# Kernel tuning notes

Hardware: AMD Instinct MI355X
Metric: run time of the kernel (lower is better)

The kernel has to match this reference:

```python
import jax, jax.numpy as jnp
import numpy as np

CONF_THRES = 0.7
IOU_THRES = 0.45
TOP_K = 1000  # max candidates kept per image after confidence filtering (YOLOv5 max_nms-style cap)
IMG_SIZE = 640.0


def _box_iou(boxes):
    """Pairwise IoU of [K,4] xyxy boxes -> [K,K]."""
    area = (boxes[:, 2] - boxes[:, 0]) * (boxes[:, 3] - boxes[:, 1])
    lt = jnp.maximum(boxes[:, None, :2], boxes[None, :, :2])
    rb = jnp.minimum(boxes[:, None, 2:], boxes[None, :, 2:])
    wh = jnp.clip(rb - lt, 0.0)
    inter = wh[..., 0] * wh[..., 1]
    return inter / (area[:, None] + area[None, :] - inter + 1e-7)


def _nms_single(pred):
    """YOLOv5-style NMS for one image. pred: [N, 9] = xywh, obj, cls_conf, pitch, yaw, roll.
    Returns fixed-shape padded detections [TOP_K, 9] and keep mask [TOP_K]."""
    obj = pred[:, 4]
    conf = obj * pred[:, 5]  # nc=1: conf = obj_conf * cls_conf
    valid = (obj > CONF_THRES) & (conf > CONF_THRES)
    score = jnp.where(valid, conf, -1.0)

    top_scores, idx = jax.lax.top_k(score, TOP_K)
    p = pred[idx]  # [TOP_K, 9]
    xy, wh = p[:, :2], p[:, 2:4]
    boxes = jnp.concatenate([xy - wh * 0.5, xy + wh * 0.5], axis=-1)  # xywh -> xyxy

    keep0 = top_scores > CONF_THRES
    iou = _box_iou(boxes)  # [TOP_K, TOP_K]
    ar = jnp.arange(TOP_K)

    # Greedy NMS: boxes are score-sorted; box j is suppressed if a kept earlier box overlaps > thresh.
    def body(i, keep):
        sup = (iou[i] > IOU_THRES) & (ar > i) & keep[i]
        return keep & (~sup)

    keep = jax.lax.fori_loop(0, TOP_K, body, keep0)

    cls = jnp.zeros((TOP_K, 1), boxes.dtype)  # single class (head)
    out = jnp.concatenate([boxes, top_scores[:, None], cls, p[:, 6:9]], axis=-1)  # [TOP_K, 9]
    out = out * keep[:, None].astype(out.dtype)  # zero padded/suppressed rows
    return out, keep


def setup_inputs() -> dict:
    key = jax.random.key(0)
    B, N = 32, 25200
    r = jax.random.uniform(key, (B, N, 9), dtype=jnp.float32)
    xy = r[..., :2] * IMG_SIZE                 # box centers in pixels
    wh = r[..., 2:4] * 128.0 + 4.0             # box sizes 4..132 px
    obj = r[..., 4:5]                          # objectness in [0,1)
    cls = r[..., 5:6] * 0.5 + 0.5              # class conf in [0.5,1)
    ang = (r[..., 6:9] - 0.5) * 2.0            # normalized pitch/yaw/roll
    prediction = jnp.concatenate([xy, wh, obj, cls, ang], axis=-1)
    return {"prediction": prediction}


def reference(prediction):
    out, keep = jax.vmap(_nms_single)(prediction)
    return out, keep
```

## Files before the change

### kernel.cpp

```cpp
#include <hip/hip_runtime.h>
#include <stdint.h>

#pragma clang fp contract(off)

#define BATCH 32
#define NPRED 25200
#define ROWF 9
#define TOPK 1000
#define SUBS 8
#define ROWS_PER_SUB (NPRED / SUBS)
#define SUBCAP 512
#define CONF_T 0.7f
#define IOU_T 0.45f
#define KW 16
#define SUPROW 1024
#define TKROW 1024

typedef unsigned long long u64;
typedef unsigned int u32;

#define WS_CAND 0
#define WS_TKEY (1048576)
#define WS_SUP  (WS_TKEY + 262144)

__device__ __forceinline__ u64 readlane64(u64 v, int l) {
    u32 lo = __builtin_amdgcn_readlane((u32)v, (u32)l);
    u32 hi = __builtin_amdgcn_readlane((u32)(v >> 32), (u32)l);
    return ((u64)hi << 32) | lo;
}

__global__ __launch_bounds__(512) void compact_sort_kernel(const float* __restrict__ pred,
                                                           u64* __restrict__ cand_ws,
                                                           u64* __restrict__ tkey_ws) {
    __shared__ float stage[512 * ROWF];
    __shared__ u64 skey[SUBCAP];
    __shared__ u32 cnt;
    int bs = blockIdx.x;
    int b = bs >> 3, s = bs & 7;
    int tid = threadIdx.x;
    if (tid == 0) cnt = 0;
    skey[tid] = 0;
    if (tid < 128) tkey_ws[bs * 128 + tid] = 0;
    __syncthreads();
    int r0 = s * ROWS_PER_SUB;
    for (int c0 = 0; c0 < ROWS_PER_SUB; c0 += 512) {
        int nrows = ROWS_PER_SUB - c0; if (nrows > 512) nrows = 512;
        int nfl = nrows * ROWF;
        size_t g0 = ((size_t)b * NPRED + r0 + c0) * ROWF;
        int h = (int)((4 - (g0 & 3)) & 3); if (h > nfl) h = nfl;
        if (tid < h) stage[tid] = pred[g0 + tid];
        int nv = (nfl - h) >> 2;
        const float4* pv = (const float4*)(pred + g0 + h);
        for (int v = tid; v < nv; v += 512) {
            float4 q = pv[v];
            int d = h + v * 4;
            stage[d] = q.x; stage[d + 1] = q.y; stage[d + 2] = q.z; stage[d + 3] = q.w;
        }
        for (int t2 = h + nv * 4 + tid; t2 < nfl; t2 += 512) stage[t2] = pred[g0 + t2];
        __syncthreads();
        if (tid < nrows) {
            float obj = stage[tid * ROWF + 4];
            float cls = stage[tid * ROWF + 5];
            float conf = obj * cls;
            if (obj > CONF_T && conf > CONF_T) {
                int r = r0 + c0 + tid;
                u32 slot = atomicAdd(&cnt, 1u);
                if (slot < SUBCAP)
                    skey[slot] = ((u64)__float_as_uint(conf) << 32) | (u64)(u32)(~(u32)r);
            }
        }
        __syncthreads();
    }
    for (int k = 2; k <= SUBCAP; k <<= 1) {
        for (int j = k >> 1; j > 0; j >>= 1) {
            int t = tid, p = t ^ j;
            if (p > t) {
                u64 a = skey[t], c2 = skey[p];
                bool desc = ((t & k) == 0);
                if (desc ? (a < c2) : (a > c2)) { skey[t] = c2; skey[p] = a; }
            }
            __syncthreads();
        }
    }
    cand_ws[(size_t)bs * SUBCAP + tid] = skey[tid];
}

__global__ __launch_bounds__(512) void rank_kernel(const u64* __restrict__ cand_ws,
                                                   u64* __restrict__ tkey_ws) {
    __shared__ u64 lists[SUBS * SUBCAP];
    int bs = blockIdx.x;
    int b = bs >> 3, s = bs & 7;
    int tid = threadIdx.x;
    const u64* src = cand_ws + (size_t)b * SUBS * SUBCAP;
    for (int t = tid; t < SUBS * SUBCAP; t += 512) lists[t] = src[t];
    __syncthreads();
    u64 key = lists[(s << 9) + tid];
    if (key) {
        int lo[SUBS];
#pragma unroll
        for (int l = 0; l < SUBS; ++l) lo[l] = 0;
#pragma unroll
        for (int w2 = SUBCAP; w2 >= 1; w2 >>= 1) {
#pragma unroll
            for (int l = 0; l < SUBS; ++l) {
                int p = lo[l] + w2;
                if (p <= SUBCAP && lists[(l << 9) + p - 1] > key) lo[l] = p;
            }
        }
        int rank = 0;
#pragma unroll
        for (int l = 0; l < SUBS; ++l) rank += lo[l];
        if (rank < TOPK) tkey_ws[(size_t)b * TKROW + rank] = key;
    }
}

__global__ __launch_bounds__(1024) void supmat_kernel(const float* __restrict__ pred,
                                                      const u64* __restrict__ tkey_ws,
                                                      u64* __restrict__ sup_g) {
    __shared__ float4 bx_s[TOPK];
    __shared__ float  ar_s[TOPK];
    int b = blockIdx.x >> 3, q = blockIdx.x & 7;
    int tid = threadIdx.x;
    if (tid < TOPK) {
        u64 key = tkey_ws[(size_t)b * TKROW + tid];
        float4 box = make_float4(0.f, 0.f, 0.f, 0.f);
        float ar = 0.f;
        if (key) {
            u32 r = ~(u32)key;
            const float* p = pred + ((size_t)b * NPRED + r) * ROWF;
            float x = p[0], y = p[1], w = p[2], hh = p[3];
            box = make_float4(x - w * 0.5f, y - hh * 0.5f, x + w * 0.5f, y + hh * 0.5f);
            ar = (box.z - box.x) * (box.w - box.y);
        }
        bx_s[tid] = box; ar_s[tid] = ar;
    }
    __syncthreads();
    int wave = tid >> 6, lane = tid & 63;
    for (int pass = 0; pass < 2; ++pass) {
        int t = (pass == 0) ? (q * 16 + wave) : ((wave == 15) ? 128 + q : 136);
        if (t >= 136) continue;
        int iw = 0, rem = t, c = 16;
        while (rem >= c) { rem -= c; c--; iw++; }
        int jw = iw + rem;
        int i = iw * 64 + lane;
        bool act = i < TOPK;
        float4 bi = act ? bx_s[i] : make_float4(0.f, 0.f, 0.f, 0.f);
        float ai = act ? ar_s[i] : 0.f;
        u64 m = 0;
        int jbase = jw << 6;
        int jend = jbase + 64; if (jend > TOPK) jend = TOPK;
        for (int j = jbase; j < jend; ++j) {
            float4 bj = bx_s[j];
            float aj = ar_s[j];
            float lx = fmaxf(bi.x, bj.x);
            float ly = fmaxf(bi.y, bj.y);
            float rx = fminf(bi.z, bj.z);
            float ry = fminf(bi.w, bj.w);
            float iw2 = rx - lx; iw2 = iw2 > 0.f ? iw2 : 0.f;
            float ih = ry - ly; ih = ih > 0.f ? ih : 0.f;
            float inter = iw2 * ih;
            float den = ai + aj - inter + 1e-7f;
            float iou = inter / den;
            if (act && j > i && iou > IOU_T) m |= 1ull << (j - jbase);
        }
        if (act) sup_g[((size_t)b * KW + jw) * SUPROW + i] = m;
    }
}

__global__ __launch_bounds__(1024) void scan_out_kernel(const float* __restrict__ pred,
                                                        const u64* __restrict__ tkey_ws,
                                                        const u64* __restrict__ sup_g,
                                                        float* __restrict__ out,
                                                        float* __restrict__ keepout) {
    __shared__ u64 keep_lds[KW];
    __shared__ u64 acc_lds;
    int b = blockIdx.x, tid = threadIdx.x;
    int w = tid >> 6, lane = tid & 63;
    const u64* S = sup_g + (size_t)b * KW * SUPROW;

    u64 key = tkey_ws[(size_t)b * TKROW + tid];
    u64 keep0 = __ballot(key != 0ull);
    if (lane == 0) keep_lds[w] = keep0;

    u64 sup_reg[KW];
    u64 diagreg = 0;
#pragma unroll
    for (int bi = 0; bi < KW; ++bi) {
        sup_reg[bi] = S[(size_t)w * SUPROW + (bi << 6) + lane];
        if (bi == w) diagreg = sup_reg[bi];
    }
    __syncthreads();

    u64 nzmask = __ballot(diagreg != 0);

#pragma unroll
    for (int bi = 0; bi < KW; ++bi) {
        if (w == bi) {
            u64 cur = keep_lds[bi];
            u64 active = cur & nzmask;
            while (active) {
                int i = __ffsll((long long)active) - 1;
                u64 wi = readlane64(diagreg, i);
                active &= active - 1;
                cur &= ~wi;
                active &= ~wi;
            }
            if (lane == 0) { keep_lds[bi] = cur; acc_lds = cur; }
        }
        __syncthreads();
        if (w > bi) {
            u64 A = acc_lds;
            u64 myv = sup_reg[bi];
            bool accb = (A >> lane) & 1ull;
            u64 lanes = __ballot(accb && myv != 0ull);
            if (lanes) {
                u64 wred = 0;
                while (lanes) {
                    int l = __ffsll((long long)lanes) - 1;
                    wred |= readlane64(myv, l);
                    lanes &= lanes - 1;
                }
                if (lane == 0) keep_lds[w] &= ~wred;
            }
        }
        __syncthreads();
    }

    if (tid < TOPK) {
        bool kp = ((keep_lds[w] >> lane) & 1ull) != 0;
        float o0 = 0.f, o1 = 0.f, o2 = 0.f, o3 = 0.f, o4 = 0.f, o6 = 0.f, o7 = 0.f, o8 = 0.f;
        if (kp) {
            u32 r = ~(u32)key;
            const float* p = pred + ((size_t)b * NPRED + r) * ROWF;
            float x = p[0], y = p[1], wd = p[2], hh = p[3];
            o0 = x - wd * 0.5f; o1 = y - hh * 0.5f;
            o2 = x + wd * 0.5f; o3 = y + hh * 0.5f;
            o4 = __uint_as_float((u32)(key >> 32));
            o6 = p[6]; o7 = p[7]; o8 = p[8];
        }
        size_t ob = ((size_t)b * TOPK + tid) * ROWF;
        out[ob + 0] = o0; out[ob + 1] = o1; out[ob + 2] = o2; out[ob + 3] = o3;
        out[ob + 4] = o4; out[ob + 5] = 0.f;
        out[ob + 6] = o6; out[ob + 7] = o7; out[ob + 8] = o8;
        keepout[(size_t)b * TOPK + tid] = kp ? 1.0f : 0.0f;
    }
}

extern "C" void kernel_launch(void* const* d_in, const int* in_sizes, int n_in,
                              void* d_out, int out_size, void* d_ws, size_t ws_size,
                              hipStream_t stream) {
    const float* pred = (const float*)d_in[0];
    float* out = (float*)d_out;
    float* keepout = out + (size_t)BATCH * TOPK * ROWF;
    char* ws = (char*)d_ws;
    u64* cand_ws = (u64*)(ws + WS_CAND);
    u64* tkey_ws = (u64*)(ws + WS_TKEY);
    u64* sup_g = (u64*)(ws + WS_SUP);

    compact_sort_kernel<<<BATCH * SUBS, 512, 0, stream>>>(pred, cand_ws, tkey_ws);
    rank_kernel<<<BATCH * SUBS, 512, 0, stream>>>(cand_ws, tkey_ws);
    supmat_kernel<<<BATCH * SUBS, 1024, 0, stream>>>(pred, tkey_ws, sup_g);
    scan_out_kernel<<<BATCH, 1024, 0, stream>>>(pred, tkey_ws, sup_g, out, keepout);
}
```

Measured before the change: 131.7 us.

## Fuse four NMS stages into one cooperative kernel with grid syncs

Merges the compaction/sort, rank-merge, suppression-matrix and greedy-scan kernels into a single cooperative launch of 256 blocks of 512 threads, separated by grid-wide barriers. Shared memory is reused across the phases, and the suppression and scan phases are remapped to 512 threads (each wave handles two 64-column chunks). The goal is to remove the inter-kernel launch gaps and the tail effects between stages. In exchange, the scan phase runs with half the threads per block, and grid.sync barriers plus cooperative launch add their own overhead.

```diff
diff --git a/kernel.cpp b/kernel.cpp
--- a/kernel.cpp
+++ b/kernel.cpp
@@ -1,5 +1,8 @@
 #include <hip/hip_runtime.h>
+#include <hip/hip_cooperative_groups.h>
 #include <stdint.h>
+
+namespace cg = cooperative_groups;
 
 #pragma clang fp contract(off)
 
@@ -29,220 +32,249 @@
     return ((u64)hi << 32) | lo;
 }
 
-__global__ __launch_bounds__(512) void compact_sort_kernel(const float* __restrict__ pred,
-                                                           u64* __restrict__ cand_ws,
-                                                           u64* __restrict__ tkey_ws) {
-    __shared__ float stage[512 * ROWF];
-    __shared__ u64 skey[SUBCAP];
+__global__ __launch_bounds__(512) void mega_kernel(const float* __restrict__ pred,
+                                                   u64* __restrict__ cand_ws,
+                                                   u64* __restrict__ tkey_ws,
+                                                   u64* __restrict__ sup_g,
+                                                   float* __restrict__ out,
+                                                   float* __restrict__ keepout) {
+    cg::grid_group grid = cg::this_grid();
+    __shared__ u64 smem[SUBS * SUBCAP];
     __shared__ u32 cnt;
+    __shared__ u64 acc_lds;
+    __shared__ u64 keep_sh[KW];
+
     int bs = blockIdx.x;
     int b = bs >> 3, s = bs & 7;
     int tid = threadIdx.x;
-    if (tid == 0) cnt = 0;
-    skey[tid] = 0;
-    if (tid < 128) tkey_ws[bs * 128 + tid] = 0;
-    __syncthreads();
-    int r0 = s * ROWS_PER_SUB;
-    for (int c0 = 0; c0 < ROWS_PER_SUB; c0 += 512) {
-        int nrows = ROWS_PER_SUB - c0; if (nrows > 512) nrows = 512;
-        int nfl = nrows * ROWF;
-        size_t g0 = ((size_t)b * NPRED + r0 + c0) * ROWF;
-        int h = (int)((4 - (g0 & 3)) & 3); if (h > nfl) h = nfl;
-        if (tid < h) stage[tid] = pred[g0 + tid];
-        int nv = (nfl - h) >> 2;
-        const float4* pv = (const float4*)(pred + g0 + h);
-        for (int v = tid; v < nv; v += 512) {
-            float4 q = pv[v];
-            int d = h + v * 4;
-            stage[d] = q.x; stage[d + 1] = q.y; stage[d + 2] = q.z; stage[d + 3] = q.w;
-        }
-        for (int t2 = h + nv * 4 + tid; t2 < nfl; t2 += 512) stage[t2] = pred[g0 + t2];
-        __syncthreads();
-        if (tid < nrows) {
-            float obj = stage[tid * ROWF + 4];
-            float cls = stage[tid * ROWF + 5];
-            float conf = obj * cls;
-            if (obj > CONF_T && conf > CONF_T) {
-                int r = r0 + c0 + tid;
-                u32 slot = atomicAdd(&cnt, 1u);
-                if (slot < SUBCAP)
-                    skey[slot] = ((u64)__float_as_uint(conf) << 32) | (u64)(u32)(~(u32)r);
-            }
-        }
-        __syncthreads();
-    }
-    for (int k = 2; k <= SUBCAP; k <<= 1) {
-        for (int j = k >> 1; j > 0; j >>= 1) {
-            int t = tid, p = t ^ j;
-            if (p > t) {
-                u64 a = skey[t], c2 = skey[p];
-                bool desc = ((t & k) == 0);
-                if (desc ? (a < c2) : (a > c2)) { skey[t] = c2; skey[p] = a; }
-            }
-            __syncthreads();
-        }
-    }
-    cand_ws[(size_t)bs * SUBCAP + tid] = skey[tid];
-}
-
-__global__ __launch_bounds__(512) void rank_kernel(const u64* __restrict__ cand_ws,
-                                                   u64* __restrict__ tkey_ws) {
-    __shared__ u64 lists[SUBS * SUBCAP];
-    int bs = blockIdx.x;
-    int b = bs >> 3, s = bs & 7;
-    int tid = threadIdx.x;
-    const u64* src = cand_ws + (size_t)b * SUBS * SUBCAP;
-    for (int t = tid; t < SUBS * SUBCAP; t += 512) lists[t] = src[t];
-    __syncthreads();
-    u64 key = lists[(s << 9) + tid];
-    if (key) {
-        int lo[SUBS];
-#pragma unroll
-        for (int l = 0; l < SUBS; ++l) lo[l] = 0;
-#pragma unroll
-        for (int w2 = SUBCAP; w2 >= 1; w2 >>= 1) {
-#pragma unroll
-            for (int l = 0; l < SUBS; ++l) {
-                int p = lo[l] + w2;
-                if (p <= SUBCAP && lists[(l << 9) + p - 1] > key) lo[l] = p;
-            }
-        }
-        int rank = 0;
-#pragma unroll
-        for (int l = 0; l < SUBS; ++l) rank += lo[l];
-        if (rank < TOPK) tkey_ws[(size_t)b * TKROW + rank] = key;
-    }
-}
-
-__global__ __launch_bounds__(1024) void supmat_kernel(const float* __restrict__ pred,
-                                                      const u64* __restrict__ tkey_ws,
-                                                      u64* __restrict__ sup_g) {
-    __shared__ float4 bx_s[TOPK];
-    __shared__ float  ar_s[TOPK];
-    int b = blockIdx.x >> 3, q = blockIdx.x & 7;
-    int tid = threadIdx.x;
-    if (tid < TOPK) {
-        u64 key = tkey_ws[(size_t)b * TKROW + tid];
-        float4 box = make_float4(0.f, 0.f, 0.f, 0.f);
-        float ar = 0.f;
+
+    {
+        float* stage = (float*)smem;
+        u64* skey = smem + 2304;
+        if (tid == 0) cnt = 0;
+        skey[tid] = 0;
+        if (tid < 128) tkey_ws[bs * 128 + tid] = 0;
+        __syncthreads();
+        int r0 = s * ROWS_PER_SUB;
+        for (int c0 = 0; c0 < ROWS_PER_SUB; c0 += 512) {
+            int nrows = ROWS_PER_SUB - c0; if (nrows > 512) nrows = 512;
+            int nfl = nrows * ROWF;
+            size_t g0 = ((size_t)b * NPRED + r0 + c0) * ROWF;
+            int h = (int)((4 - (g0 & 3)) & 3); if (h > nfl) h = nfl;
+            if (tid < h) stage[tid] = pred[g0 + tid];
+            int nv = (nfl - h) >> 2;
+            const float4* pv = (const float4*)(pred + g0 + h);
+            for (int v = tid; v < nv; v += 512) {
+                float4 q = pv[v];
+                int d = h + v * 4;
+                stage[d] = q.x; stage[d + 1] = q.y; stage[d + 2] = q.z; stage[d + 3] = q.w;
+            }
+            for (int t2 = h + nv * 4 + tid; t2 < nfl; t2 += 512) stage[t2] = pred[g0 + t2];
+            __syncthreads();
+            if (tid < nrows) {
+                float obj = stage[tid * ROWF + 4];
+                float cls = stage[tid * ROWF + 5];
+                float conf = obj * cls;
+                if (obj > CONF_T && conf > CONF_T) {
+                    int r = r0 + c0 + tid;
+                    u32 slot = atomicAdd(&cnt, 1u);
+                    if (slot < SUBCAP)
+                        skey[slot] = ((u64)__float_as_uint(conf) << 32) | (u64)(u32)(~(u32)r);
+                }
+            }
+            __syncthreads();
+        }
+        for (int k = 2; k <= SUBCAP; k <<= 1) {
+            for (int j = k >> 1; j > 0; j >>= 1) {
+                int t = tid, p = t ^ j;
+                if (p > t) {
+                    u64 a = skey[t], c2 = skey[p];
+                    bool desc = ((t & k) == 0);
+                    if (desc ? (a < c2) : (a > c2)) { skey[t] = c2; skey[p] = a; }
+                }
+                __syncthreads();
+            }
+        }
+        cand_ws[(size_t)bs * SUBCAP + tid] = skey[tid];
+    }
+    __threadfence();
+    grid.sync();
+
+    {
+        u64* lists = smem;
+        const u64* src = cand_ws + (size_t)b * SUBS * SUBCAP;
+        for (int t = tid; t < SUBS * SUBCAP; t += 512) lists[t] = src[t];
+        __syncthreads();
+        u64 key = lists[(s << 9) + tid];
         if (key) {
-            u32 r = ~(u32)key;
-            const float* p = pred + ((size_t)b * NPRED + r) * ROWF;
-            float x = p[0], y = p[1], w = p[2], hh = p[3];
-            box = make_float4(x - w * 0.5f, y - hh * 0.5f, x + w * 0.5f, y + hh * 0.5f);
-            ar = (box.z - box.x) * (box.w - box.y);
-        }
-        bx_s[tid] = box; ar_s[tid] = ar;
-    }
-    __syncthreads();
-    int wave = tid >> 6, lane = tid & 63;
-    for (int pass = 0; pass < 2; ++pass) {
-        int t = (pass == 0) ? (q * 16 + wave) : ((wave == 15) ? 128 + q : 136);
-        if (t >= 136) continue;
-        int iw = 0, rem = t, c = 16;
-        while (rem >= c) { rem -= c; c--; iw++; }
-        int jw = iw + rem;
-        int i = iw * 64 + lane;
-        bool act = i < TOPK;
-        float4 bi = act ? bx_s[i] : make_float4(0.f, 0.f, 0.f, 0.f);
-        float ai = act ? ar_s[i] : 0.f;
-        u64 m = 0;
-        int jbase = jw << 6;
-        int jend = jbase + 64; if (jend > TOPK) jend = TOPK;
-        for (int j = jbase; j < jend; ++j) {
-            float4 bj = bx_s[j];
-            float aj = ar_s[j];
-            float lx = fmaxf(bi.x, bj.x);
-            float ly = fmaxf(bi.y, bj.y);
-            float rx = fminf(bi.z, bj.z);
-            float ry = fminf(bi.w, bj.w);
-            float iw2 = rx - lx; iw2 = iw2 > 0.f ? iw2 : 0.f;
-            float ih = ry - ly; ih = ih > 0.f ? ih : 0.f;
-            float inter = iw2 * ih;
-            float den = ai + aj - inter + 1e-7f;
-            float iou = inter / den;
-            if (act && j > i && iou > IOU_T) m |= 1ull << (j - jbase);
-        }
-        if (act) sup_g[((size_t)b * KW + jw) * SUPROW + i] = m;
-    }
-}
-
-__global__ __launch_bounds__(1024) void scan_out_kernel(const float* __restrict__ pred,
-                                                        const u64* __restrict__ tkey_ws,
-                                                        const u64* __restrict__ sup_g,
-                                                        float* __restrict__ out,
-                                                        float* __restrict__ keepout) {
-    __shared__ u64 keep_lds[KW];
-    __shared__ u64 acc_lds;
-    int b = blockIdx.x, tid = threadIdx.x;
-    int w = tid >> 6, lane = tid & 63;
-    const u64* S = sup_g + (size_t)b * KW * SUPROW;
-
-    u64 key = tkey_ws[(size_t)b * TKROW + tid];
-    u64 keep0 = __ballot(key != 0ull);
-    if (lane == 0) keep_lds[w] = keep0;
-
-    u64 sup_reg[KW];
-    u64 diagreg = 0;
-#pragma unroll
-    for (int bi = 0; bi < KW; ++bi) {
-        sup_reg[bi] = S[(size_t)w * SUPROW + (bi << 6) + lane];
-        if (bi == w) diagreg = sup_reg[bi];
-    }
-    __syncthreads();
-
-    u64 nzmask = __ballot(diagreg != 0);
-
-#pragma unroll
-    for (int bi = 0; bi < KW; ++bi) {
-        if (w == bi) {
-            u64 cur = keep_lds[bi];
-            u64 active = cur & nzmask;
-            while (active) {
-                int i = __ffsll((long long)active) - 1;
-                u64 wi = readlane64(diagreg, i);
-                active &= active - 1;
-                cur &= ~wi;
-                active &= ~wi;
-            }
-            if (lane == 0) { keep_lds[bi] = cur; acc_lds = cur; }
-        }
-        __syncthreads();
-        if (w > bi) {
+            int lo[SUBS];
+#pragma unroll
+            for (int l = 0; l < SUBS; ++l) lo[l] = 0;
+#pragma unroll
+            for (int w2 = SUBCAP; w2 >= 1; w2 >>= 1) {
+#pragma unroll
+                for (int l = 0; l < SUBS; ++l) {
+                    int p = lo[l] + w2;
+                    if (p <= SUBCAP && lists[(l << 9) + p - 1] > key) lo[l] = p;
+                }
+            }
+            int rank = 0;
+#pragma unroll
+            for (int l = 0; l < SUBS; ++l) rank += lo[l];
+            if (rank < TOPK) tkey_ws[(size_t)b * TKROW + rank] = key;
+        }
+    }
+    __threadfence();
+    grid.sync();
+
+    {
+        float4* bx_s = (float4*)smem;
+        float* ar_s = (float*)(smem + 2000);
+        for (int t = tid; t < TOPK; t += 512) {
+            u64 key = tkey_ws[(size_t)b * TKROW + t];
+            float4 box = make_float4(0.f, 0.f, 0.f, 0.f);
+            float ar = 0.f;
+            if (key) {
+                u32 r = ~(u32)key;
+                const float* p = pred + ((size_t)b * NPRED + r) * ROWF;
+                float x = p[0], y = p[1], w = p[2], hh = p[3];
+                box = make_float4(x - w * 0.5f, y - hh * 0.5f, x + w * 0.5f, y + hh * 0.5f);
+                ar = (box.z - box.x) * (box.w - box.y);
+            }
+            bx_s[t] = box; ar_s[t] = ar;
+        }
+        __syncthreads();
+        int w = tid >> 6, lane = tid & 63;
+        int gw = (s << 3) + w;
+        for (int ti = 0; ti < 3; ++ti) {
+            int t = gw + (ti << 6);
+            if (t >= 136) break;
+            int iw = 0, rem = t, c = 16;
+            while (rem >= c) { rem -= c; c--; iw++; }
+            int jw = iw + rem;
+            int i = iw * 64 + lane;
+            bool act = i < TOPK;
+            float4 bi = act ? bx_s[i] : make_float4(0.f, 0.f, 0.f, 0.f);
+            float ai = act ? ar_s[i] : 0.f;
+            u64 m = 0;
+            int jbase = jw << 6;
+            int jend = jbase + 64; if (jend > TOPK) jend = TOPK;
+            for (int j = jbase; j < jend; ++j) {
+                float4 bj = bx_s[j];
+                float aj = ar_s[j];
+                float lx = fmaxf(bi.x, bj.x);
+                float ly = fmaxf(bi.y, bj.y);
+                float rx = fminf(bi.z, bj.z);
+                float ry = fminf(bi.w, bj.w);
+                float iw2 = rx - lx; iw2 = iw2 > 0.f ? iw2 : 0.f;
+                float ih = ry - ly; ih = ih > 0.f ? ih : 0.f;
+                float inter = iw2 * ih;
+                float den = ai + aj - inter + 1e-7f;
+                float iou = inter / den;
+                if (act && j > i && iou > IOU_T) m |= 1ull << (j - jbase);
+            }
+            if (act) sup_g[((size_t)b * KW + jw) * SUPROW + i] = m;
+        }
+    }
+    __threadfence();
+    grid.sync();
+
+    if (bs < BATCH) {
+        int bb = bs;
+        int w = tid >> 6, lane = tid & 63;
+        int cA = w, cB = w + 8;
+        const u64* S = sup_g + (size_t)bb * KW * SUPROW;
+
+        u64 keyA = tkey_ws[(size_t)bb * TKROW + tid];
+        u64 keyB = tkey_ws[(size_t)bb * TKROW + 512 + tid];
+        u64 k0A = __ballot(keyA != 0ull);
+        u64 k0B = __ballot(keyB != 0ull);
+        if (lane == 0) { keep_sh[w] = k0A; keep_sh[w + 8] = k0B; }
+
+        u64 regA[8], regB[KW];
+#pragma unroll
+        for (int bi = 0; bi < 8; ++bi)
+            regA[bi] = S[(size_t)cA * SUPROW + (bi << 6) + lane];
+#pragma unroll
+        for (int bi = 0; bi < KW; ++bi)
+            regB[bi] = S[(size_t)cB * SUPROW + (bi << 6) + lane];
+        u64 diagA = S[(size_t)cA * SUPROW + (cA << 6) + lane];
+        u64 diagB = S[(size_t)cB * SUPROW + (cB << 6) + lane];
+        __syncthreads();
+        u64 nzA = __ballot(diagA != 0ull);
+        u64 nzB = __ballot(diagB != 0ull);
+
+#pragma unroll
+        for (int bi = 0; bi < KW; ++bi) {
+            if (w == (bi & 7)) {
+                u64 diag = (bi < 8) ? diagA : diagB;
+                u64 nz = (bi < 8) ? nzA : nzB;
+                u64 cur = keep_sh[bi];
+                u64 active = cur & nz;
+                while (active) {
+                    int i = __ffsll((long long)active) - 1;
+                    u64 wi = readlane64(diag, i);
+                    active &= active - 1;
+                    cur &= ~wi;
+                    active &= ~wi;
+                }
+                if (lane == 0) { keep_sh[bi] = cur; acc_lds = cur; }
+            }
+            __syncthreads();
             u64 A = acc_lds;
-            u64 myv = sup_reg[bi];
-            bool accb = (A >> lane) & 1ull;
-            u64 lanes = __ballot(accb && myv != 0ull);
-            if (lanes) {
-                u64 wred = 0;
-                while (lanes) {
-                    int l = __ffsll((long long)lanes) - 1;
-                    wred |= readlane64(myv, l);
-                    lanes &= lanes - 1;
-                }
-                if (lane == 0) keep_lds[w] &= ~wred;
-            }
-        }
-        __syncthreads();
-    }
-
-    if (tid < TOPK) {
-        bool kp = ((keep_lds[w] >> lane) & 1ull) != 0;
-        float o0 = 0.f, o1 = 0.f, o2 = 0.f, o3 = 0.f, o4 = 0.f, o6 = 0.f, o7 = 0.f, o8 = 0.f;
-        if (kp) {
-            u32 r = ~(u32)key;
-            const float* p = pred + ((size_t)b * NPRED + r) * ROWF;
-            float x = p[0], y = p[1], wd = p[2], hh = p[3];
-            o0 = x - wd * 0.5f; o1 = y - hh * 0.5f;
-            o2 = x + wd * 0.5f; o3 = y + hh * 0.5f;
-            o4 = __uint_as_float((u32)(key >> 32));
-            o6 = p[6]; o7 = p[7]; o8 = p[8];
-        }
-        size_t ob = ((size_t)b * TOPK + tid) * ROWF;
-        out[ob + 0] = o0; out[ob + 1] = o1; out[ob + 2] = o2; out[ob + 3] = o3;
-        out[ob + 4] = o4; out[ob + 5] = 0.f;
-        out[ob + 6] = o6; out[ob + 7] = o7; out[ob + 8] = o8;
-        keepout[(size_t)b * TOPK + tid] = kp ? 1.0f : 0.0f;
+            bool accb = ((A >> lane) & 1ull) != 0;
+            if (bi < 8 && cA > bi) {
+                u64 myv = regA[bi];
+                u64 lanes = __ballot(accb && myv != 0ull);
+                if (lanes) {
+                    u64 wred = 0;
+                    while (lanes) {
+                        int l = __ffsll((long long)lanes) - 1;
+                        wred |= readlane64(myv, l);
+                        lanes &= lanes - 1;
+                    }
+                    if (lane == 0) keep_sh[cA] &= ~wred;
+                }
+            }
+            if (cB > bi) {
+                u64 myv = regB[bi];
+                u64 lanes = __ballot(accb && myv != 0ull);
+                if (lanes) {
+                    u64 wred = 0;
+                    while (lanes) {
+                        int l = __ffsll((long long)lanes) - 1;
+                        wred |= readlane64(myv, l);
+                        lanes &= lanes - 1;
+                    }
+                    if (lane == 0) keep_sh[cB] &= ~wred;
+                }
+            }
+            __syncthreads();
+        }
+
+#pragma unroll
+        for (int pass = 0; pass < 2; ++pass) {
+            int row = tid + (pass << 9);
+            u64 key = pass ? keyB : keyA;
+            if (row < TOPK) {
+                bool kp = ((keep_sh[row >> 6] >> (row & 63)) & 1ull) != 0;
+                float o0 = 0.f, o1 = 0.f, o2 = 0.f, o3 = 0.f, o4 = 0.f, o6 = 0.f, o7 = 0.f, o8 = 0.f;
+                if (kp) {
+                    u32 r = ~(u32)key;
+                    const float* p = pred + ((size_t)bb * NPRED + r) * ROWF;
+                    float x = p[0], y = p[1], wd = p[2], hh = p[3];
+                    o0 = x - wd * 0.5f; o1 = y - hh * 0.5f;
+                    o2 = x + wd * 0.5f; o3 = y + hh * 0.5f;
+                    o4 = __uint_as_float((u32)(key >> 32));
+                    o6 = p[6]; o7 = p[7]; o8 = p[8];
+                }
+                size_t ob = ((size_t)bb * TOPK + row) * ROWF;
+                out[ob + 0] = o0; out[ob + 1] = o1; out[ob + 2] = o2; out[ob + 3] = o3;
+                out[ob + 4] = o4; out[ob + 5] = 0.f;
+                out[ob + 6] = o6; out[ob + 7] = o7; out[ob + 8] = o8;
+                keepout[(size_t)bb * TOPK + row] = kp ? 1.0f : 0.0f;
+            }
+        }
     }
 }
 
@@ -257,8 +289,8 @@
     u64* tkey_ws = (u64*)(ws + WS_TKEY);
     u64* sup_g = (u64*)(ws + WS_SUP);
 
-    compact_sort_kernel<<<BATCH * SUBS, 512, 0, stream>>>(pred, cand_ws, tkey_ws);
-    rank_kernel<<<BATCH * SUBS, 512, 0, stream>>>(cand_ws, tkey_ws);
-    supmat_kernel<<<BATCH * SUBS, 1024, 0, stream>>>(pred, tkey_ws, sup_g);
-    scan_out_kernel<<<BATCH, 1024, 0, stream>>>(pred, tkey_ws, sup_g, out, keepout);
+    void* args[] = { (void*)&pred, (void*)&cand_ws, (void*)&tkey_ws,
+                     (void*)&sup_g, (void*)&out, (void*)&keepout };
+    hipLaunchCooperativeKernel((void*)mega_kernel, dim3(BATCH * SUBS), dim3(512),
+                               args, 0, stream);
 }
```

New measurement: 318.0 us. 2.42x slower.

## Fuse suppression-matrix build and greedy scan into one LDS-resident kernel

Applied to the files above, without the earlier changes.

Merges the IoU suppression-mask kernel and the scan/output kernel into one per-image kernel. The mask matrix is kept in shared memory with a padded stride instead of going through global workspace. This removes a kernel launch and the global write/read of the matrix. In exchange, the IoU work now runs on only one block per image rather than eight, which reduces parallelism and raises LDS use per block.

```diff
diff --git a/kernel.cpp b/kernel.cpp
--- a/kernel.cpp
+++ b/kernel.cpp
@@ -13,15 +13,14 @@
 #define CONF_T 0.7f
 #define IOU_T 0.45f
 #define KW 16
-#define SUPROW 1024
 #define TKROW 1024
+#define LSTRIDE 1001
 
 typedef unsigned long long u64;
 typedef unsigned int u32;
 
 #define WS_CAND 0
 #define WS_TKEY (1048576)
-#define WS_SUP  (WS_TKEY + 262144)
 
 __device__ __forceinline__ u64 readlane64(u64 v, int l) {
     u32 lo = __builtin_amdgcn_readlane((u32)v, (u32)l);
@@ -114,31 +113,36 @@
     }
 }
 
-__global__ __launch_bounds__(1024) void supmat_kernel(const float* __restrict__ pred,
-                                                      const u64* __restrict__ tkey_ws,
-                                                      u64* __restrict__ sup_g) {
+__global__ __launch_bounds__(1024) void supscan_kernel(const float* __restrict__ pred,
+                                                       const u64* __restrict__ tkey_ws,
+                                                       float* __restrict__ out,
+                                                       float* __restrict__ keepout) {
+    __shared__ u64 supc[KW * LSTRIDE];
     __shared__ float4 bx_s[TOPK];
     __shared__ float  ar_s[TOPK];
-    int b = blockIdx.x >> 3, q = blockIdx.x & 7;
-    int tid = threadIdx.x;
-    if (tid < TOPK) {
-        u64 key = tkey_ws[(size_t)b * TKROW + tid];
+    __shared__ u64 keep_sh[KW];
+    __shared__ u64 acc_lds;
+    int b = blockIdx.x, tid = threadIdx.x;
+    int w = tid >> 6, lane = tid & 63;
+
+    u64 key = tkey_ws[(size_t)b * TKROW + tid];
+    {
         float4 box = make_float4(0.f, 0.f, 0.f, 0.f);
         float ar = 0.f;
         if (key) {
             u32 r = ~(u32)key;
             const float* p = pred + ((size_t)b * NPRED + r) * ROWF;
-            float x = p[0], y = p[1], w = p[2], hh = p[3];
-            box = make_float4(x - w * 0.5f, y - hh * 0.5f, x + w * 0.5f, y + hh * 0.5f);
+            float x = p[0], y = p[1], wd = p[2], hh = p[3];
+            box = make_float4(x - wd * 0.5f, y - hh * 0.5f, x + wd * 0.5f, y + hh * 0.5f);
             ar = (box.z - box.x) * (box.w - box.y);
         }
-        bx_s[tid] = box; ar_s[tid] = ar;
-    }
-    __syncthreads();
-    int wave = tid >> 6, lane = tid & 63;
-    for (int pass = 0; pass < 2; ++pass) {
-        int t = (pass == 0) ? (q * 16 + wave) : ((wave == 15) ? 128 + q : 136);
-        if (t >= 136) continue;
+        if (tid < TOPK) { bx_s[tid] = box; ar_s[tid] = ar; }
+        u64 k0 = __ballot(key != 0ull);
+        if (lane == 0) keep_sh[w] = k0;
+    }
+    __syncthreads();
+
+    for (int t = w; t < 136; t += 16) {
         int iw = 0, rem = t, c = 16;
         while (rem >= c) { rem -= c; c--; iw++; }
         int jw = iw + rem;
@@ -163,40 +167,21 @@
             float iou = inter / den;
             if (act && j > i && iou > IOU_T) m |= 1ull << (j - jbase);
         }
-        if (act) sup_g[((size_t)b * KW + jw) * SUPROW + i] = m;
-    }
-}
-
-__global__ __launch_bounds__(1024) void scan_out_kernel(const float* __restrict__ pred,
-                                                        const u64* __restrict__ tkey_ws,
-                                                        const u64* __restrict__ sup_g,
-                                                        float* __restrict__ out,
-                                                        float* __restrict__ keepout) {
-    __shared__ u64 keep_lds[KW];
-    __shared__ u64 acc_lds;
-    int b = blockIdx.x, tid = threadIdx.x;
-    int w = tid >> 6, lane = tid & 63;
-    const u64* S = sup_g + (size_t)b * KW * SUPROW;
-
-    u64 key = tkey_ws[(size_t)b * TKROW + tid];
-    u64 keep0 = __ballot(key != 0ull);
-    if (lane == 0) keep_lds[w] = keep0;
+        if (act) supc[jw * LSTRIDE + i] = m;
+    }
+    __syncthreads();
 
     u64 sup_reg[KW];
-    u64 diagreg = 0;
-#pragma unroll
-    for (int bi = 0; bi < KW; ++bi) {
-        sup_reg[bi] = S[(size_t)w * SUPROW + (bi << 6) + lane];
-        if (bi == w) diagreg = sup_reg[bi];
-    }
-    __syncthreads();
-
-    u64 nzmask = __ballot(diagreg != 0);
+#pragma unroll
+    for (int bi = 0; bi < KW; ++bi)
+        sup_reg[bi] = supc[w * LSTRIDE + (bi << 6) + lane];
+    u64 diagreg = supc[w * LSTRIDE + (w << 6) + lane];
+    u64 nzmask = __ballot(diagreg != 0ull);
 
 #pragma unroll
     for (int bi = 0; bi < KW; ++bi) {
         if (w == bi) {
-            u64 cur = keep_lds[bi];
+            u64 cur = keep_sh[bi];
             u64 active = cur & nzmask;
             while (active) {
                 int i = __ffsll((long long)active) - 1;
@@ -205,13 +190,13 @@
                 cur &= ~wi;
                 active &= ~wi;
             }
-            if (lane == 0) { keep_lds[bi] = cur; acc_lds = cur; }
+            if (lane == 0) { keep_sh[bi] = cur; acc_lds = cur; }
         }
         __syncthreads();
         if (w > bi) {
             u64 A = acc_lds;
             u64 myv = sup_reg[bi];
-            bool accb = (A >> lane) & 1ull;
+            bool accb = ((A >> lane) & 1ull) != 0;
             u64 lanes = __ballot(accb && myv != 0ull);
             if (lanes) {
                 u64 wred = 0;
@@ -220,14 +205,14 @@
                     wred |= readlane64(myv, l);
                     lanes &= lanes - 1;
                 }
-                if (lane == 0) keep_lds[w] &= ~wred;
+                if (lane == 0) keep_sh[w] &= ~wred;
             }
         }
         __syncthreads();
     }
 
     if (tid < TOPK) {
-        bool kp = ((keep_lds[w] >> lane) & 1ull) != 0;
+        bool kp = ((keep_sh[w] >> lane) & 1ull) != 0;
         float o0 = 0.f, o1 = 0.f, o2 = 0.f, o3 = 0.f, o4 = 0.f, o6 = 0.f, o7 = 0.f, o8 = 0.f;
         if (kp) {
             u32 r = ~(u32)key;
@@ -255,10 +240,8 @@
     char* ws = (char*)d_ws;
     u64* cand_ws = (u64*)(ws + WS_CAND);
     u64* tkey_ws = (u64*)(ws + WS_TKEY);
-    u64* sup_g = (u64*)(ws + WS_SUP);
 
     compact_sort_kernel<<<BATCH * SUBS, 512, 0, stream>>>(pred, cand_ws, tkey_ws);
     rank_kernel<<<BATCH * SUBS, 512, 0, stream>>>(cand_ws, tkey_ws);
-    supmat_kernel<<<BATCH * SUBS, 1024, 0, stream>>>(pred, tkey_ws, sup_g);
-    scan_out_kernel<<<BATCH, 1024, 0, stream>>>(pred, tkey_ws, sup_g, out, keepout);
-}
+    supscan_kernel<<<BATCH, 1024, 0, stream>>>(pred, tkey_ws, out, keepout);
+}
```

Result: slower. 225.1 us (+70.9%).
